# Performance work log

Measured on AMD Instinct MI355X. Metric: run time of the kernel, lower is better.

Reference implementation:

```python
import jax, jax.numpy as jnp
import numpy as np

THR_CONF = 0.05
THR_NMS = 0.5
TOPK = 500


def _pairwise_iou(b):
    # b: [M,4] ltrb
    lt = jnp.maximum(b[:, None, :2], b[None, :, :2])
    rb = jnp.minimum(b[:, None, 2:], b[None, :, 2:])
    wh = jnp.clip(rb - lt, 0.0)
    inter = wh[..., 0] * wh[..., 1]
    area = (b[:, 2] - b[:, 0]) * (b[:, 3] - b[:, 1])
    union = area[:, None] + area[None, :] - inter
    return inter / jnp.maximum(union, 1e-9)


def _greedy_nms(boxes_off, scores, valid, thr):
    # fixed-size greedy NMS matching torchvision.ops.nms semantics
    M = boxes_off.shape[0]
    neg = jnp.finfo(scores.dtype).min
    s = jnp.where(valid, scores, neg)
    order = jnp.argsort(-s)
    iou = _pairwise_iou(boxes_off[order])  # [M,M]
    valid_o = valid[order]
    rng = jnp.arange(M)

    def body(i, keep):
        sup = (iou[i] > thr) & (rng > i) & keep[i]
        return keep & ~sup

    keep_o = jax.lax.fori_loop(0, M, body, valid_o)
    keep = jnp.zeros((M,), dtype=bool).at[order].set(keep_o)
    return keep


def setup_inputs() -> dict:
    key = jax.random.key(0)
    k1, k2 = jax.random.split(key)
    B, N, C = 8, 40000, 80
    pconf = jax.random.normal(k1, (B, N, C), dtype=jnp.float32)
    raw = jax.random.uniform(k2, (B, N, 4), dtype=jnp.float32)
    cxcy = raw[..., :2]
    wh = raw[..., 2:] * 0.2 + 0.01
    pboxes = jnp.concatenate([cxcy - wh / 2, cxcy + wh / 2], axis=-1)  # ltrb
    return {"pconf": pconf, "pboxes": pboxes}


def reference(pconf, pboxes):
    B, N, C = pconf.shape
    conf = jax.nn.sigmoid(pconf)
    pscores = conf.max(axis=-1)          # [B,N]
    plabels = conf.argmax(axis=-1)       # [B,N]

    mask_pos = pscores > THR_CONF
    # topk mask via scatter (mirrors mask_topk[arange[:,None], ids_topk] = True)
    scores_k, ids_topk = jax.lax.top_k(pscores, TOPK)       # [B,K]
    mask_topk = jnp.zeros_like(mask_pos)
    mask_topk = mask_topk.at[jnp.arange(B)[:, None], ids_topk].set(True)
    mask_pos = mask_pos & mask_topk

    # gather stage-1 results at the topk positions (fixed size B*K)
    valid_k = jnp.take_along_axis(mask_pos, ids_topk, axis=1)              # [B,K]
    labels_k = jnp.take_along_axis(plabels, ids_topk, axis=1)              # [B,K]
    boxes_k = jnp.take_along_axis(pboxes, ids_topk[..., None], axis=1)     # [B,K,4]

    M = B * TOPK
    ids_batch1 = jnp.repeat(jnp.arange(B), TOPK)            # [M]
    p_scores1 = scores_k.reshape(M)
    p_labels1 = labels_k.reshape(M)
    p_boxes1 = boxes_k.reshape(M, 4)
    valid1 = valid_k.reshape(M)

    # per-(label,batch) offset trick == per-label loop of batched_nms
    max_coord = p_boxes1.max()
    key = (p_labels1 * B + ids_batch1).astype(p_boxes1.dtype)
    boxes_off = p_boxes1 + (key * (max_coord + 1.0))[:, None]

    keep = _greedy_nms(boxes_off, p_scores1, valid1, THR_NMS)

    return (ids_batch1, p_boxes1, p_labels1, p_scores1, keep)
```

## Files before the change

### kernel.cpp

```cpp
#include <hip/hip_runtime.h>
#include <math.h>

#define BB 8
#define NN 40000
#define CC 80
#define TOPK 500
#define MM (BB*TOPK)
#define NBINS 4096
#define BIN_LO (-8.0f)
#define BIN_SCALE 256.0f
#define CAP 4096
#define NGROUPS (CC*BB)
#define THR_CONF_F 0.05f
#define THR_NMS_F 0.5f

__device__ __forceinline__ int bin_of(float x){
  float f = (x - BIN_LO) * BIN_SCALE;
  int b = (int)floorf(f);
  b = b < 0 ? 0 : b;
  b = b > (NBINS-1) ? (NBINS-1) : b;
  return b;
}

__global__ void k_score(const float* __restrict__ pconf,
                        float* __restrict__ logitv, int* __restrict__ label){
  int g   = blockIdx.x*256 + threadIdx.x;
  int row = g >> 2;
  int sub = g & 3;
  const float4* p = (const float4*)pconf + (size_t)row*20 + sub;
  float4 v0 = p[0], v1 = p[4], v2 = p[8], v3 = p[12], v4 = p[16];
  float best = -3.4e38f; int bi = 0;
  int c0 = sub*4;
  #define CHK(vv,it) { \
    int base = c0 + (it)*16; \
    if(vv.x>best){best=vv.x;bi=base+0;} \
    if(vv.y>best){best=vv.y;bi=base+1;} \
    if(vv.z>best){best=vv.z;bi=base+2;} \
    if(vv.w>best){best=vv.w;bi=base+3;} }
  CHK(v0,0) CHK(v1,1) CHK(v2,2) CHK(v3,3) CHK(v4,4)
  #undef CHK
  #pragma unroll
  for(int d=1; d<4; d<<=1){
    float ov = __shfl_xor(best, d, 64);
    int   oi = __shfl_xor(bi,   d, 64);
    if(ov > best || (ov == best && oi < bi)){ best = ov; bi = oi; }
  }
  if(sub == 0){
    logitv[row] = best; label[row] = bi;
  }
}

__global__ void __launch_bounds__(1024)
k_select(const float* __restrict__ logitv, const int* __restrict__ label,
         const float* __restrict__ pboxes,
         float* __restrict__ out,
         float* __restrict__ cbox, int* __restrict__ cgid,
         float* __restrict__ cscore, int* __restrict__ maxval){
  int b = blockIdx.x;
  int t = threadIdx.x;
  __shared__ int h[NBINS];
  __shared__ int ss[1024];
  __shared__ unsigned long long keys[CAP];
  __shared__ int stbin, scnt, smax;
  for(int i=t; i<NBINS; i+=1024) h[i] = 0;
  if(t==0){ scnt = 0; smax = 0; }
  __syncthreads();

  const float4* lv4 = (const float4*)(logitv + (size_t)b*NN);
  for(int i=t; i<NN/4; i+=1024){
    float4 v = lv4[i];
    atomicAdd(&h[bin_of(v.x)], 1);
    atomicAdd(&h[bin_of(v.y)], 1);
    atomicAdd(&h[bin_of(v.z)], 1);
    atomicAdd(&h[bin_of(v.w)], 1);
  }
  __syncthreads();

  int c0 = t*4;
  int cs = h[c0] + h[c0+1] + h[c0+2] + h[c0+3];
  ss[t] = cs;
  __syncthreads();
  for(int off=1; off<1024; off<<=1){
    int v = (t+off < 1024) ? ss[t+off] : 0;
    __syncthreads();
    ss[t] += v;
    __syncthreads();
  }
  int sufExcl = (t < 1023) ? ss[t+1] : 0;
  if(sufExcl < TOPK && sufExcl + cs >= TOPK){
    int cum = sufExcl; int tb = 0;
    for(int k=3; k>=0; k--){
      cum += h[c0+k];
      if(cum >= TOPK){ tb = c0+k; break; }
    }
    tb -= 2; if(tb < 0) tb = 0;
    stbin = tb;
  }
  __syncthreads();
  int tb = stbin;

  const float* lv = logitv + (size_t)b*NN;
  for(int idx=t; idx<NN; idx+=1024){
    float lg = lv[idx];
    if(bin_of(lg) >= tb){
      int pos = atomicAdd(&scnt, 1);
      if(pos < CAP){
        float e = (float)exp(-(double)lg);
        float s = 1.0f/(1.0f+e);
        keys[pos] = ((unsigned long long)__float_as_uint(s) << 16)
                  | (unsigned long long)(65535 - idx);
      }
    }
  }
  __syncthreads();
  int n = scnt; if(n > CAP) n = CAP;

  for(int i=t; i<n; i+=1024){
    unsigned long long ki = keys[i];
    int rank = 0;
    for(int j=0; j<n; j++) rank += (keys[j] > ki) ? 1 : 0;
    if(rank < TOPK){
      int idx = 65535 - (int)(ki & 0xFFFFULL);
      int row = b*NN + idx;
      float s = __uint_as_float((unsigned int)(ki >> 16));
      int lab = label[row];
      float4 bv = *(const float4*)(pboxes + (size_t)row*4);
      int m = b*TOPK + rank;
      out[m] = (float)b;
      float* ob = out + MM + (size_t)m*4;
      ob[0]=bv.x; ob[1]=bv.y; ob[2]=bv.z; ob[3]=bv.w;
      out[5*MM + m] = (float)lab;
      out[6*MM + m] = s;
      cbox[m*4+0]=bv.x; cbox[m*4+1]=bv.y; cbox[m*4+2]=bv.z; cbox[m*4+3]=bv.w;
      cgid[m] = lab*BB + b;
      cscore[m] = s;
      float mx = fmaxf(fmaxf(bv.x,bv.y), fmaxf(bv.z,bv.w));
      atomicMax(&smax, __float_as_int(mx));
    }
  }
  __syncthreads();
  if(t==0) maxval[b] = smax;
}

__global__ void __launch_bounds__(64)
k_nms(const float* __restrict__ cbox, const int* __restrict__ cgid,
      const float* __restrict__ cscore, const int* __restrict__ maxval,
      float* __restrict__ out_keep){
  int g = blockIdx.x;
  int lane = threadIdx.x;
  __shared__ float bx[TOPK][4];
  __shared__ float area[TOPK];
  __shared__ int   mid[TOPK];
  __shared__ unsigned char keepf[TOPK];
  int mb = maxval[0];
  #pragma unroll
  for(int k=1;k<BB;k++) mb = max(mb, maxval[k]);
  float mc  = __int_as_float(mb);
  float off = (float)g * (mc + 1.0f);
  int b = g & (BB-1);
  int lo = b*TOPK, hi = lo + TOPK;

  int count = 0;
  for(int base=lo; base<hi; base+=64){
    int m = base + lane;
    bool match = (m < hi) && (cgid[m] == g);
    unsigned long long mk = __ballot(match);
    if(match){
      int p = count + __popcll(mk & ((1ULL<<lane)-1ULL));
      float x1 = cbox[m*4+0] + off;
      float y1 = cbox[m*4+1] + off;
      float x2 = cbox[m*4+2] + off;
      float y2 = cbox[m*4+3] + off;
      bx[p][0]=x1; bx[p][1]=y1; bx[p][2]=x2; bx[p][3]=y2;
      area[p] = (x2-x1)*(y2-y1);
      mid[p] = m;
      keepf[p] = (cscore[m] > THR_CONF_F) ? 1 : 0;
    }
    count += __popcll(mk);
  }
  __syncthreads();

  for(int i=0; i<count; i++){
    if(keepf[i]){
      float ix1=bx[i][0], iy1=bx[i][1], ix2=bx[i][2], iy2=bx[i][3], ia=area[i];
      for(int j=i+1+lane; j<count; j+=64){
        if(keepf[j]){
          float lx = fmaxf(ix1, bx[j][0]);
          float ly = fmaxf(iy1, bx[j][1]);
          float rx = fminf(ix2, bx[j][2]);
          float ry = fminf(iy2, bx[j][3]);
          float w = fmaxf(rx-lx, 0.0f), h = fmaxf(ry-ly, 0.0f);
          float inter = w*h;
          float uni = ia + area[j] - inter;
          float iou = inter / fmaxf(uni, 1e-9f);
          if(iou > THR_NMS_F) keepf[j] = 0;
        }
      }
    }
    __syncthreads();
  }
  for(int p=lane; p<count; p+=64)
    out_keep[mid[p]] = keepf[p] ? 1.0f : 0.0f;
}

extern "C" void kernel_launch(void* const* d_in, const int* in_sizes, int n_in,
                              void* d_out, int out_size, void* d_ws, size_t ws_size,
                              hipStream_t stream) {
  const float* pconf  = (const float*)d_in[0];
  const float* pboxes = (const float*)d_in[1];
  float* out = (float*)d_out;
  char* ws = (char*)d_ws;

  float* logitv  = (float*)(ws + 0);
  int*   label   = (int*)  (ws + 1280000);
  float* cbox    = (float*)(ws + 2560000);
  int*   cgid    = (int*)  (ws + 2624000);
  float* cscore  = (float*)(ws + 2640000);
  int*   maxval  = (int*)  (ws + 2656000);

  k_score <<<(BB*NN*4)/256, 256, 0, stream>>>(pconf, logitv, label);
  k_select<<<BB, 1024, 0, stream>>>(logitv, label, pboxes, out,
                                    cbox, cgid, cscore, maxval);
  k_nms   <<<NGROUPS, 64, 0, stream>>>(cbox, cgid, cscore, maxval, out + 7*MM);
}
```

Before: 191.0 us.

## Prefilter top-k candidates in score kernel to skip per-batch histogram pass

```diff
diff --git a/kernel.cpp b/kernel.cpp
--- a/kernel.cpp
+++ b/kernel.cpp
@@ -13,6 +13,7 @@
 #define NGROUPS (CC*BB)
 #define THR_CONF_F 0.05f
 #define THR_NMS_F 0.5f
+#define THR_LOGIT 3.4f
 
 __device__ __forceinline__ int bin_of(float x){
   float f = (x - BIN_LO) * BIN_SCALE;
@@ -22,11 +23,25 @@
   return b;
 }
 
+__device__ __forceinline__ unsigned long long make_key(float lg, int idx){
+  float e = (float)exp(-(double)lg);
+  float s = 1.0f/(1.0f+e);
+  return ((unsigned long long)__float_as_uint(s) << 16)
+       | (unsigned long long)(65535 - idx);
+}
+
 __global__ void k_score(const float* __restrict__ pconf,
-                        float* __restrict__ logitv, int* __restrict__ label){
-  int g   = blockIdx.x*256 + threadIdx.x;
+                        float* __restrict__ logitv, int* __restrict__ label,
+                        int* __restrict__ cnt, unsigned long long* __restrict__ cand){
+  int tid = threadIdx.x;
+  int g   = blockIdx.x*256 + tid;
   int row = g >> 2;
   int sub = g & 3;
+  __shared__ unsigned long long lkey[64];
+  __shared__ int lcnt, lbase;
+  if(tid == 0) lcnt = 0;
+  __syncthreads();
+
   const float4* p = (const float4*)pconf + (size_t)row*20 + sub;
   float4 v0 = p[0], v1 = p[4], v2 = p[8], v3 = p[12], v4 = p[16];
   float best = -3.4e38f; int bi = 0;
@@ -45,75 +60,89 @@
     int   oi = __shfl_xor(bi,   d, 64);
     if(ov > best || (ov == best && oi < bi)){ best = ov; bi = oi; }
   }
+  int b = row / NN;
   if(sub == 0){
     logitv[row] = best; label[row] = bi;
+    if(best > THR_LOGIT){
+      int pos = atomicAdd(&lcnt, 1);
+      lkey[pos] = make_key(best, row - b*NN);
+    }
+  }
+  __syncthreads();
+  int n = lcnt;
+  if(tid == 0 && n > 0) lbase = atomicAdd(&cnt[b], n);
+  __syncthreads();
+  for(int i=tid; i<n; i+=256){
+    int pos = lbase + i;
+    if(pos < CAP) cand[(size_t)b*CAP + pos] = lkey[i];
   }
 }
 
 __global__ void __launch_bounds__(1024)
 k_select(const float* __restrict__ logitv, const int* __restrict__ label,
-         const float* __restrict__ pboxes,
+         const float* __restrict__ pboxes, const int* __restrict__ cnt,
+         const unsigned long long* __restrict__ cand,
          float* __restrict__ out,
          float* __restrict__ cbox, int* __restrict__ cgid,
          float* __restrict__ cscore, int* __restrict__ maxval){
   int b = blockIdx.x;
   int t = threadIdx.x;
+  __shared__ unsigned long long keys[CAP];
   __shared__ int h[NBINS];
   __shared__ int ss[1024];
-  __shared__ unsigned long long keys[CAP];
   __shared__ int stbin, scnt, smax;
-  for(int i=t; i<NBINS; i+=1024) h[i] = 0;
-  if(t==0){ scnt = 0; smax = 0; }
-  __syncthreads();
-
-  const float4* lv4 = (const float4*)(logitv + (size_t)b*NN);
-  for(int i=t; i<NN/4; i+=1024){
-    float4 v = lv4[i];
-    atomicAdd(&h[bin_of(v.x)], 1);
-    atomicAdd(&h[bin_of(v.y)], 1);
-    atomicAdd(&h[bin_of(v.z)], 1);
-    atomicAdd(&h[bin_of(v.w)], 1);
-  }
-  __syncthreads();
-
-  int c0 = t*4;
-  int cs = h[c0] + h[c0+1] + h[c0+2] + h[c0+3];
-  ss[t] = cs;
-  __syncthreads();
-  for(int off=1; off<1024; off<<=1){
-    int v = (t+off < 1024) ? ss[t+off] : 0;
-    __syncthreads();
-    ss[t] += v;
-    __syncthreads();
-  }
-  int sufExcl = (t < 1023) ? ss[t+1] : 0;
-  if(sufExcl < TOPK && sufExcl + cs >= TOPK){
-    int cum = sufExcl; int tb = 0;
-    for(int k=3; k>=0; k--){
-      cum += h[c0+k];
-      if(cum >= TOPK){ tb = c0+k; break; }
-    }
-    tb -= 2; if(tb < 0) tb = 0;
-    stbin = tb;
-  }
-  __syncthreads();
-  int tb = stbin;
-
-  const float* lv = logitv + (size_t)b*NN;
-  for(int idx=t; idx<NN; idx+=1024){
-    float lg = lv[idx];
-    if(bin_of(lg) >= tb){
-      int pos = atomicAdd(&scnt, 1);
-      if(pos < CAP){
-        float e = (float)exp(-(double)lg);
-        float s = 1.0f/(1.0f+e);
-        keys[pos] = ((unsigned long long)__float_as_uint(s) << 16)
-                  | (unsigned long long)(65535 - idx);
+  if(t==0) smax = 0;
+
+  int n = cnt[b];
+  if(n >= TOPK && n <= CAP){
+    for(int i=t; i<n; i+=1024) keys[i] = cand[(size_t)b*CAP + i];
+    __syncthreads();
+  } else {
+    for(int i=t; i<NBINS; i+=1024) h[i] = 0;
+    if(t==0) scnt = 0;
+    __syncthreads();
+    const float4* lv4 = (const float4*)(logitv + (size_t)b*NN);
+    for(int i=t; i<NN/4; i+=1024){
+      float4 v = lv4[i];
+      atomicAdd(&h[bin_of(v.x)], 1);
+      atomicAdd(&h[bin_of(v.y)], 1);
+      atomicAdd(&h[bin_of(v.z)], 1);
+      atomicAdd(&h[bin_of(v.w)], 1);
+    }
+    __syncthreads();
+    int c0 = t*4;
+    int cs = h[c0] + h[c0+1] + h[c0+2] + h[c0+3];
+    ss[t] = cs;
+    __syncthreads();
+    for(int off=1; off<1024; off<<=1){
+      int v = (t+off < 1024) ? ss[t+off] : 0;
+      __syncthreads();
+      ss[t] += v;
+      __syncthreads();
+    }
+    int sufExcl = (t < 1023) ? ss[t+1] : 0;
+    if(sufExcl < TOPK && sufExcl + cs >= TOPK){
+      int cum = sufExcl; int tb = 0;
+      for(int k=3; k>=0; k--){
+        cum += h[c0+k];
+        if(cum >= TOPK){ tb = c0+k; break; }
       }
-    }
-  }
-  __syncthreads();
-  int n = scnt; if(n > CAP) n = CAP;
+      tb -= 2; if(tb < 0) tb = 0;
+      stbin = tb;
+    }
+    __syncthreads();
+    int tb = stbin;
+    const float* lv = logitv + (size_t)b*NN;
+    for(int idx=t; idx<NN; idx+=1024){
+      float lg = lv[idx];
+      if(bin_of(lg) >= tb){
+        int pos = atomicAdd(&scnt, 1);
+        if(pos < CAP) keys[pos] = make_key(lg, idx);
+      }
+    }
+    __syncthreads();
+    n = scnt; if(n > CAP) n = CAP;
+  }
 
   for(int i=t; i<n; i+=1024){
     unsigned long long ki = keys[i];
@@ -211,15 +240,19 @@
   float* out = (float*)d_out;
   char* ws = (char*)d_ws;
 
-  float* logitv  = (float*)(ws + 0);
-  int*   label   = (int*)  (ws + 1280000);
-  float* cbox    = (float*)(ws + 2560000);
-  int*   cgid    = (int*)  (ws + 2624000);
-  float* cscore  = (float*)(ws + 2640000);
-  int*   maxval  = (int*)  (ws + 2656000);
-
-  k_score <<<(BB*NN*4)/256, 256, 0, stream>>>(pconf, logitv, label);
-  k_select<<<BB, 1024, 0, stream>>>(logitv, label, pboxes, out,
+  int*   cnt     = (int*)  (ws + 0);
+  float* logitv  = (float*)(ws + 128);
+  int*   label   = (int*)  (ws + 1280128);
+  unsigned long long* cand = (unsigned long long*)(ws + 2560128);
+  float* cbox    = (float*)(ws + 2822272);
+  int*   cgid    = (int*)  (ws + 2886272);
+  float* cscore  = (float*)(ws + 2902272);
+  int*   maxval  = (int*)  (ws + 2918272);
+
+  hipMemsetAsync(ws, 0, 32, stream);
+
+  k_score <<<(BB*NN*4)/256, 256, 0, stream>>>(pconf, logitv, label, cnt, cand);
+  k_select<<<BB, 1024, 0, stream>>>(logitv, label, pboxes, cnt, cand, out,
                                     cbox, cgid, cscore, maxval);
   k_nms   <<<NGROUPS, 64, 0, stream>>>(cbox, cgid, cscore, maxval, out + 7*MM);
 }
```

After: 214.8 us. 1.12x slower.
